# Performance work log

Hardware: AMD Instinct MI355X
Metric: run time of the kernel (lower is better)

## Reference

```python
import jax, jax.numpy as jnp
import numpy as np

D_MODEL = 1024
N_HEADS = 16
D_KV = 64
N_CONTEXT = 20
PASSAGE_LEN = 200
BSZ = 8
QLEN = 32
KLEN = N_CONTEXT * PASSAGE_LEN


def setup_inputs() -> dict:
    key = jax.random.key(0)
    ks = jax.random.split(key, 8)
    inp = {
        "input": jax.random.normal(ks[0], (BSZ, QLEN, D_MODEL), jnp.float32),
        "kv": jax.random.normal(ks[1], (BSZ, KLEN, D_MODEL), jnp.float32),
        "mask_add": jnp.zeros((BSZ, 1, 1, KLEN), jnp.float32),
        "mask_bool": jnp.ones((BSZ, 1, 1, KLEN), bool),
        "position_bias": jax.random.normal(ks[2], (1, N_HEADS, QLEN, KLEN), jnp.float32),
        "Wq": jax.random.normal(ks[3], (D_MODEL, N_HEADS * D_KV), jnp.float32) * 0.02,
        "Wk": jax.random.normal(ks[4], (D_MODEL, N_HEADS * D_KV), jnp.float32) * 0.02,
        "Wv": jax.random.normal(ks[5], (D_MODEL, N_HEADS * D_KV), jnp.float32) * 0.02,
        "Wo": jax.random.normal(ks[6], (N_HEADS * D_KV, D_MODEL), jnp.float32) * 0.02,
        "n_context": N_CONTEXT,
    }
    return inp


def reference(input, kv, mask_add, mask_bool, position_bias, Wq, Wk, Wv, Wo, n_context):
    b, qlen, dm = input.shape
    klen = kv.shape[1]
    H = position_bias.shape[1]
    dh = Wq.shape[1] // H
    # projections, [b, h, len, dh]
    q = (input @ Wq).reshape(b, qlen, H, dh).transpose(0, 2, 1, 3)
    k = (kv @ Wk).reshape(b, klen, H, dh).transpose(0, 2, 1, 3)
    v = (kv @ Wv).reshape(b, klen, H, dh).transpose(0, 2, 1, 3)
    # unscaled T5-style attention scores + additive mask + position bias
    scores = jnp.einsum('bhqd,bhkd->bhqk', q, k) + mask_add + position_bias
    attn = jax.nn.softmax(scores.astype(jnp.float32), axis=-1).astype(scores.dtype)
    # dropout p=0 (eval) -> identity
    out = jnp.einsum('bhqk,bhkd->bhqd', attn, v)
    out = out.transpose(0, 2, 1, 3).reshape(b, qlen, H * dh) @ Wo
    # collect_cross_attention(sum_over_tokens=True): masked avg of raw scores per context
    s = scores.reshape(b, H, qlen, n_context, -1)
    m = mask_bool.reshape(b, 1, 1, n_context, -1).astype(scores.dtype)
    collected = (s * m).sum(-1) / m.sum(-1)  # [b, H, qlen, n_context]
    return out, collected
```

## Files before the change

kernel.cpp:

```cpp
#include <hip/hip_runtime.h>
#include <stdint.h>

constexpr int DMODEL = 1024;
constexpr int NH     = 16;
constexpr int DHD    = 64;
constexpr int BS     = 8;
constexpr int QLEN   = 32;
constexpr int KLEN   = 4000;
constexpr int NCTX   = 20;
constexpr int PLEN   = 200;

typedef __bf16 bf16_t;
typedef bf16_t bf16x8 __attribute__((ext_vector_type(8)));
typedef float  f32x4  __attribute__((ext_vector_type(4)));

__device__ __forceinline__ uint16_t f2bf(float f) {
  uint32_t u = __float_as_uint(f);
  u += 0x7FFF + ((u >> 16) & 1);
  return (uint16_t)(u >> 16);
}

#define GLOAD_LDS16(gsrc, ldst) \
  __builtin_amdgcn_global_load_lds((const __attribute__((address_space(1))) void*)(gsrc), \
                                   (__attribute__((address_space(3))) void*)(ldst), 16, 0, 0)

__global__ void cast_inputs(const float* __restrict__ kv, const float* __restrict__ inp,
                            uint16_t* __restrict__ kv16, uint16_t* __restrict__ in16,
                            const uint32_t* __restrict__ maskw, int* __restrict__ flag) {
  if (blockIdx.x == 0 && threadIdx.x == 0)
    *flag = (maskw[0] == 0x01010101u) ? 1 : 0;
  const int NKV4 = (BS * KLEN * DMODEL) / 4;
  const int NIN4 = (BS * QLEN * DMODEL) / 4;
  const int total = NKV4 + NIN4;
  for (int i = blockIdx.x * blockDim.x + threadIdx.x; i < total; i += gridDim.x * blockDim.x) {
    float4 v; uint16_t* dst; int di;
    if (i < NKV4) { v = ((const float4*)kv)[i]; dst = kv16; di = i; }
    else          { v = ((const float4*)inp)[i - NKV4]; dst = in16; di = i - NKV4; }
    ushort4 o; o.x = f2bf(v.x); o.y = f2bf(v.y); o.z = f2bf(v.z); o.w = f2bf(v.w);
    ((ushort4*)dst)[di] = o;
  }
}

__global__ void wtrans(const float* __restrict__ w0, const float* __restrict__ w1,
                       const float* __restrict__ w2, const float* __restrict__ w3,
                       uint16_t* __restrict__ out) {
  __shared__ uint16_t sm[64][65];
  const float* W = (blockIdx.z == 0) ? w0 : (blockIdx.z == 1) ? w1 : (blockIdx.z == 2) ? w2 : w3;
  uint16_t* o = out + (size_t)blockIdx.z * DMODEL * DMODEL;
  int k0 = blockIdx.y * 64, n0 = blockIdx.x * 64;
  int t = threadIdx.x;
  for (int i = 0; i < 16; ++i) {
    int s = t + i * 256; int r = s >> 6, c = s & 63;
    sm[r][c] = f2bf(W[(size_t)(k0 + r) * DMODEL + n0 + c]);
  }
  __syncthreads();
  for (int i = 0; i < 16; ++i) {
    int s = t + i * 256; int r = s >> 6, c = s & 63;
    o[(size_t)(n0 + r) * DMODEL + k0 + c] = sm[c][r];
  }
}

template <int OUT_F32>
__global__ void __launch_bounds__(256) gemm_bt(const uint16_t* __restrict__ A,
                                               const uint16_t* __restrict__ Bt,
                                               void* __restrict__ Cv,
                                               int M, int N, int K) {
  __shared__ __align__(16) uint16_t As[128 * 32];
  __shared__ __align__(16) uint16_t Bs[64 * 32];
  const int m0 = blockIdx.x * 128, n0 = blockIdx.y * 64;
  const int tid = threadIdx.x, lane = tid & 63, wave = tid >> 6;
  const int wm = wave >> 1, wn = wave & 1;
  const int l15 = lane & 15, g = lane >> 4;
  const int sr = lane >> 2, sc = (lane & 3) * 8;
  const int c0 = wave * 3, c1 = c0 + 1, c2 = c0 + 2;
  f32x4 acc[4][2] = {};
  const int KT = K / 32;
  for (int kt = 0; kt < KT; ++kt) {
    __syncthreads();
#pragma unroll
    for (int cq = 0; cq < 3; ++cq) {
      const int c = wave * 3 + cq;
      if (c < 8)
        GLOAD_LDS16(A  + (size_t)(m0 + c * 16 + sr) * K + kt * 32 + sc, As + c * 512);
      else
        GLOAD_LDS16(Bt + (size_t)(n0 + (c - 8) * 16 + sr) * K + kt * 32 + sc, Bs + (c - 8) * 512);
    }
    __syncthreads();
    bf16x8 a[4], b[2];
#pragma unroll
    for (int i = 0; i < 4; ++i)
      a[i] = *(const bf16x8*)&As[(wm * 64 + i * 16 + l15) * 32 + g * 8];
#pragma unroll
    for (int j = 0; j < 2; ++j)
      b[j] = *(const bf16x8*)&Bs[(wn * 32 + j * 16 + l15) * 32 + g * 8];
#pragma unroll
    for (int i = 0; i < 4; ++i)
#pragma unroll
      for (int j = 0; j < 2; ++j)
        acc[i][j] = __builtin_amdgcn_mfma_f32_16x16x32_bf16(a[i], b[j], acc[i][j], 0, 0, 0);
  }
#pragma unroll
  for (int i = 0; i < 4; ++i)
#pragma unroll
    for (int j = 0; j < 2; ++j) {
      int row = m0 + wm * 64 + i * 16 + g * 4;
      int col = n0 + wn * 32 + j * 16 + l15;
      if (OUT_F32) {
        float* C = (float*)Cv;
#pragma unroll
        for (int r = 0; r < 4; ++r) C[(size_t)(row + r) * N + col] = acc[i][j][r];
      } else {
        uint16_t* C = (uint16_t*)Cv;
#pragma unroll
        for (int r = 0; r < 4; ++r) C[(size_t)(row + r) * N + col] = f2bf(acc[i][j][r]);
      }
    }
}

__global__ void __launch_bounds__(512) gemm_kv(const uint16_t* __restrict__ A,
                                               const uint16_t* __restrict__ Bt,
                                               uint16_t* __restrict__ kmat,
                                               uint16_t* __restrict__ vt) {
  __shared__ __align__(16) uint16_t smem[65536];
  const int orig = blockIdx.x;
  const int swz  = (orig & 7) * 125 + (orig >> 3);
  const int mb = swz >> 3, nb = swz & 7;
  const int m0 = mb * 256, n0 = nb * 256;
  const int tid = threadIdx.x, lane = tid & 63, wid = tid >> 6;
  const int wm = wid >> 2, wn = wid & 3;
  const int l15 = lane & 15, g = lane >> 4;
  const int l3 = lane >> 3, l7 = lane & 7;
  const int cg = (l7 ^ (l3 & 7)) * 8;

  f32x4 acc[8][4] = {};

#define ABASE(bf) (smem + (bf) * 32768)
#define BBASE(bf) (smem + (bf) * 32768 + 16384)

  auto STAGE = [&](int bf, int kt) {
    const int colg = kt * 64 + cg;
#pragma unroll
    for (int ia = 0; ia < 4; ++ia) {
      const int r0 = wid * 32 + ia * 8;
      GLOAD_LDS16(A + (size_t)(m0 + r0 + l3) * 1024 + colg, ABASE(bf) + r0 * 64);
    }
#pragma unroll
    for (int ib = 0; ib < 4; ++ib) {
      const int r0 = wid * 32 + ib * 8;
      GLOAD_LDS16(Bt + (size_t)(n0 + r0 + l3) * 1024 + colg, BBASE(bf) + r0 * 64);
    }
  };

  STAGE(0, 0);
  for (int kt = 0; kt < 16; ++kt) {
    const int bf = kt & 1;
    if (kt < 15) {
      STAGE(bf ^ 1, kt + 1);
      asm volatile("s_waitcnt vmcnt(8)" ::: "memory");
    } else {
      asm volatile("s_waitcnt vmcnt(0)" ::: "memory");
    }
    asm volatile("s_barrier" ::: "memory");
#pragma unroll
    for (int kk = 0; kk < 2; ++kk) {
      bf16x8 af[8], bb[4];
#pragma unroll
      for (int mi = 0; mi < 8; ++mi) {
        const int row = wm * 128 + mi * 16 + l15;
        const int gr = (kk * 4 + g) ^ (row & 7);
        af[mi] = *(const bf16x8*)&ABASE(bf)[row * 64 + gr * 8];
      }
#pragma unroll
      for (int ni = 0; ni < 4; ++ni) {
        const int row = wn * 64 + ni * 16 + l15;
        const int gr = (kk * 4 + g) ^ (row & 7);
        bb[ni] = *(const bf16x8*)&BBASE(bf)[row * 64 + gr * 8];
      }
#pragma unroll
      for (int mi = 0; mi < 8; ++mi)
#pragma unroll
        for (int ni = 0; ni < 4; ++ni)
          acc[mi][ni] = __builtin_amdgcn_mfma_f32_16x16x32_bf16(af[mi], bb[ni], acc[mi][ni], 0, 0, 0);
    }
    asm volatile("s_barrier" ::: "memory");
  }
#undef ABASE
#undef BBASE

  if (n0 < 1024) {
#pragma unroll
    for (int mi = 0; mi < 8; ++mi)
#pragma unroll
      for (int ni = 0; ni < 4; ++ni) {
        const int row = m0 + wm * 128 + mi * 16 + g * 4;
        const int col = n0 + wn * 64 + ni * 16 + l15;
#pragma unroll
        for (int r = 0; r < 4; ++r)
          kmat[(size_t)(row + r) * 1024 + col] = f2bf(acc[mi][ni][r]);
      }
  } else {
#pragma unroll
    for (int mi = 0; mi < 8; ++mi)
#pragma unroll
      for (int ni = 0; ni < 4; ++ni) {
        const int dd = wn * 64 + ni * 16 + l15;
        const int kk_tok = wm * 128 + mi * 16 + g * 4;
#pragma unroll
        for (int r = 0; r < 4; ++r)
          smem[dd * 256 + kk_tok + r] = f2bf(acc[mi][ni][r]);
      }
    __syncthreads();
    const int hbase = (n0 - 1024) >> 6;
#pragma unroll
    for (int it = 0; it < 16; ++it) {
      const int sp = it * 512 + tid;
      const int dd = sp >> 5, kk0 = (sp & 31) * 8;
      const int grow = m0 + kk0;
      const int b = grow / 4000, krel = grow - b * 4000;
      const int h = hbase + (dd >> 6), d = dd & 63;
      ulonglong2 v = *(const ulonglong2*)&smem[dd * 256 + kk0];
      *(ulonglong2*)&vt[(((size_t)(b * NH + h) * DHD + d) * KLEN) + krel] = v;
    }
  }
}

__global__ void __launch_bounds__(256) fused_attn(const uint16_t* __restrict__ Q,
                                                  const uint16_t* __restrict__ Km,
                                                  const uint16_t* __restrict__ Vt,
                                                  const float* __restrict__ mask_add,
                                                  const void* __restrict__ maskb,
                                                  const int* __restrict__ flag,
                                                  const float* __restrict__ bias,
                                                  float* __restrict__ part,
                                                  float* __restrict__ coll) {
  __shared__ __align__(16) uint16_t plds[4][32 * 32];
  const int kc = blockIdx.x, h = blockIdx.y, b = blockIdx.z;
  const int lane = threadIdx.x & 63, wave = threadIdx.x >> 6;
  const int l15 = lane & 15, g = lane >> 4;
  const int ctx = kc * 4 + wave;
  const int kbase = ctx * PLEN;
  const int fm = *flag;

  bf16x8 aq[2][2];
#pragma unroll
  for (int i = 0; i < 2; ++i)
#pragma unroll
    for (int ks = 0; ks < 2; ++ks)
      aq[i][ks] = *(const bf16x8*)&Q[(size_t)(b * QLEN + i * 16 + l15) * DMODEL + h * DHD + ks * 32 + g * 8];

  f32x4 o[2][4] = {};
  float mr[2][4], lr[2][4], cs[2][4];
#pragma unroll
  for (int i = 0; i < 2; ++i)
#pragma unroll
    for (int r = 0; r < 4; ++r) { mr[i][r] = -3e38f; lr[i][r] = 0.f; cs[i][r] = 0.f; }
  float cnt = 0.f;

  for (int t = 0; t < 7; ++t) {
    const int k0 = kbase + t * 32;
    bf16x8 kb[2][2];
#pragma unroll
    for (int j = 0; j < 2; ++j) {
      int kr = k0 + j * 16 + l15; if (kr > KLEN - 1) kr = KLEN - 1;
#pragma unroll
      for (int ks = 0; ks < 2; ++ks)
        kb[j][ks] = *(const bf16x8*)&Km[(size_t)(b * KLEN + kr) * DMODEL + h * DHD + ks * 32 + g * 8];
    }
    f32x4 sa[2][2] = {};
#pragma unroll
    for (int ks = 0; ks < 2; ++ks)
#pragma unroll
      for (int i = 0; i < 2; ++i)
#pragma unroll
        for (int j = 0; j < 2; ++j)
          sa[i][j] = __builtin_amdgcn_mfma_f32_16x16x32_bf16(aq[i][ks], kb[j][ks], sa[i][j], 0, 0, 0);

    int colc[2]; bool vd[2], vm[2]; float ma[2];
#pragma unroll
    for (int j = 0; j < 2; ++j) {
      int col = k0 + j * 16 + l15;
      vd[j] = (col < kbase + PLEN);
      int cc = col; if (cc > KLEN - 1) cc = KLEN - 1;
      colc[j] = cc;
      ma[j] = mask_add[b * KLEN + cc];
      bool mk = fm ? (((const uint8_t*)maskb)[b * KLEN + cc] != 0)
                   : (((const int*)maskb)[b * KLEN + cc] != 0);
      vm[j] = vd[j] && mk;
    }

    float sv[2][2][4];
    float tmax[2][4];
#pragma unroll
    for (int i = 0; i < 2; ++i)
#pragma unroll
      for (int r = 0; r < 4; ++r) {
        tmax[i][r] = -3e38f;
        const int q = i * 16 + g * 4 + r;
        const size_t brow = (size_t)(h * QLEN + q) * KLEN;
#pragma unroll
        for (int j = 0; j < 2; ++j) {
          float raw = sa[i][j][r] + ma[j] + bias[brow + colc[j]];
          cs[i][r] += vm[j] ? raw : 0.f;
          float x = vd[j] ? raw : -3e38f;
          sv[i][j][r] = x;
          tmax[i][r] = fmaxf(tmax[i][r], x);
        }
      }
#pragma unroll
    for (int j = 0; j < 2; ++j) cnt += vm[j] ? 1.f : 0.f;

#pragma unroll
    for (int i = 0; i < 2; ++i)
#pragma unroll
      for (int r = 0; r < 4; ++r) {
        float v = tmax[i][r];
        v = fmaxf(v, __shfl_xor(v, 1)); v = fmaxf(v, __shfl_xor(v, 2));
        v = fmaxf(v, __shfl_xor(v, 4)); v = fmaxf(v, __shfl_xor(v, 8));
        tmax[i][r] = v;
      }
    float scale[2][4];
#pragma unroll
    for (int i = 0; i < 2; ++i)
#pragma unroll
      for (int r = 0; r < 4; ++r) {
        float mn = fmaxf(mr[i][r], tmax[i][r]);
        scale[i][r] = __expf(mr[i][r] - mn);
        mr[i][r] = mn;
        lr[i][r] *= scale[i][r];
      }
#pragma unroll
    for (int i = 0; i < 2; ++i)
#pragma unroll
      for (int j2 = 0; j2 < 4; ++j2)
#pragma unroll
        for (int r = 0; r < 4; ++r)
          o[i][j2][r] *= scale[i][r];
#pragma unroll
    for (int i = 0; i < 2; ++i)
#pragma unroll
      for (int r = 0; r < 4; ++r) {
        const int q = i * 16 + g * 4 + r;
#pragma unroll
        for (int j = 0; j < 2; ++j) {
          float p = __expf(sv[i][j][r] - mr[i][r]);
          lr[i][r] += p;
          plds[wave][q * 32 + j * 16 + l15] = f2bf(p);
        }
      }
    bf16x8 ap[2];
#pragma unroll
    for (int i = 0; i < 2; ++i)
      ap[i] = *(const bf16x8*)&plds[wave][(i * 16 + l15) * 32 + g * 8];
    bf16x8 vb[4];
    int vc = k0 + g * 8; if (vc > KLEN - 8) vc = KLEN - 8;
#pragma unroll
    for (int j2 = 0; j2 < 4; ++j2)
      vb[j2] = *(const bf16x8*)&Vt[((size_t)((b * NH + h) * DHD + j2 * 16 + l15)) * KLEN + vc];
#pragma unroll
    for (int i = 0; i < 2; ++i)
#pragma unroll
      for (int j2 = 0; j2 < 4; ++j2)
        o[i][j2] = __builtin_amdgcn_mfma_f32_16x16x32_bf16(ap[i], vb[j2], o[i][j2], 0, 0, 0);
  }

#pragma unroll
  for (int i = 0; i < 2; ++i)
#pragma unroll
    for (int r = 0; r < 4; ++r) {
      float v = lr[i][r];
      v += __shfl_xor(v, 1); v += __shfl_xor(v, 2); v += __shfl_xor(v, 4); v += __shfl_xor(v, 8);
      lr[i][r] = v;
      float c = cs[i][r];
      c += __shfl_xor(c, 1); c += __shfl_xor(c, 2); c += __shfl_xor(c, 4); c += __shfl_xor(c, 8);
      cs[i][r] = c;
    }
  { float c = cnt; c += __shfl_xor(c, 1); c += __shfl_xor(c, 2); c += __shfl_xor(c, 4); c += __shfl_xor(c, 8); cnt = c; }

  float* pr = part + ((size_t)((b * NH + h) * NCTX + ctx)) * 32 * 72;
#pragma unroll
  for (int i = 0; i < 2; ++i)
#pragma unroll
    for (int j2 = 0; j2 < 4; ++j2)
#pragma unroll
      for (int r = 0; r < 4; ++r)
        pr[(i * 16 + g * 4 + r) * 72 + 8 + j2 * 16 + l15] = o[i][j2][r];
  if (l15 == 0) {
#pragma unroll
    for (int i = 0; i < 2; ++i)
#pragma unroll
      for (int r = 0; r < 4; ++r) {
        int q = i * 16 + g * 4 + r;
        pr[q * 72 + 0] = mr[i][r];
        pr[q * 72 + 1] = lr[i][r];
        coll[(((size_t)(b * NH + h)) * QLEN + q) * NCTX + ctx] = cs[i][r] / cnt;
      }
  }
}

__global__ void __launch_bounds__(256) combine_attn(const float* __restrict__ part,
                                                    uint16_t* __restrict__ ao16) {
  const int t = threadIdx.x;
  const int row = blockIdx.x * 16 + (t >> 4);
  const int ln = t & 15;
  const int bh = row >> 5, q = row & 31;
  const float* p0 = part + ((size_t)bh * 640 + q) * 72;
  float M = -3e38f;
#pragma unroll
  for (int c = 0; c < NCTX; ++c) M = fmaxf(M, p0[(size_t)c * 2304]);
  float Z = 0.f, o0 = 0.f, o1 = 0.f, o2 = 0.f, o3 = 0.f;
  const int d0 = ln * 4;
  for (int c = 0; c < NCTX; ++c) {
    const float* pc = p0 + (size_t)c * 2304;
    float e = __expf(pc[0] - M);
    Z += e * pc[1];
    float4 ov = *(const float4*)&pc[8 + d0];
    o0 += e * ov.x; o1 += e * ov.y; o2 += e * ov.z; o3 += e * ov.w;
  }
  float iz = 1.f / Z;
  const int b = bh >> 4, h = bh & 15;
  ushort4 w; w.x = f2bf(o0 * iz); w.y = f2bf(o1 * iz); w.z = f2bf(o2 * iz); w.w = f2bf(o3 * iz);
  *(ushort4*)&ao16[(size_t)(b * QLEN + q) * DMODEL + h * DHD + d0] = w;
}

extern "C" void kernel_launch(void* const* d_in, const int* in_sizes, int n_in,
                              void* d_out, int out_size, void* d_ws, size_t ws_size,
                              hipStream_t stream) {
  const float* input     = (const float*)d_in[0];
  const float* kv        = (const float*)d_in[1];
  const float* mask_add  = (const float*)d_in[2];
  const void*  mask_bool = d_in[3];
  const float* bias      = (const float*)d_in[4];
  const float* Wq        = (const float*)d_in[5];
  const float* Wk        = (const float*)d_in[6];
  const float* Wv        = (const float*)d_in[7];
  const float* Wo        = (const float*)d_in[8];
  float* out  = (float*)d_out;
  float* coll = out + (size_t)BS * QLEN * DMODEL;

  char* ws = (char*)d_ws;
  size_t off = 0;
  auto alloc = [&](size_t bytes) { char* p = ws + off; off += (bytes + 255) & ~(size_t)255; return p; };
  uint16_t* kv16 = (uint16_t*)alloc((size_t)BS * KLEN * DMODEL * 2);
  uint16_t* in16 = (uint16_t*)alloc((size_t)BS * QLEN * DMODEL * 2);
  uint16_t* wt   = (uint16_t*)alloc((size_t)4 * DMODEL * DMODEL * 2);
  uint16_t* q16  = (uint16_t*)alloc((size_t)BS * QLEN * DMODEL * 2);
  uint16_t* kmat = (uint16_t*)alloc((size_t)BS * KLEN * DMODEL * 2);
  uint16_t* vt   = (uint16_t*)alloc((size_t)BS * KLEN * DMODEL * 2);
  float*    part = (float*)   alloc((size_t)BS * NH * NCTX * 32 * 72 * 4);
  uint16_t* ao16 = (uint16_t*)alloc((size_t)BS * QLEN * DMODEL * 2);
  int*      flag = (int*)alloc(256);

  uint16_t* WqT  = wt;
  uint16_t* WkvT = wt + (size_t)DMODEL * DMODEL;
  uint16_t* WoT  = wt + (size_t)3 * DMODEL * DMODEL;

  cast_inputs<<<2048, 256, 0, stream>>>(kv, input, kv16, in16,
                                        (const uint32_t*)mask_bool, flag);
  wtrans<<<dim3(16, 16, 4), 256, 0, stream>>>(Wq, Wk, Wv, Wo, wt);
  gemm_bt<0><<<dim3(2, 16), 256, 0, stream>>>(in16, WqT, q16, BS * QLEN, DMODEL, DMODEL);
  gemm_kv<<<1000, 512, 0, stream>>>(kv16, WkvT, kmat, vt);
  fused_attn<<<dim3(5, NH, BS), 256, 0, stream>>>(q16, kmat, vt, mask_add, mask_bool, flag,
                                                  bias, part, coll);
  combine_attn<<<256, 256, 0, stream>>>(part, ao16);
  gemm_bt<1><<<dim3(2, 16), 256, 0, stream>>>(ao16, WoT, out, BS * QLEN, DMODEL, DMODEL);
}
```

Baseline: 287.8 us.

## Split each context across two waves and merge partial softmax in LDS

Each passage of 200 keys is now processed by two waves of 100 keys each, and the grid doubles from 5 to 10 blocks along the context axis. The two halves' running max, sum, output accumulators and masked score sums are merged through shared memory before one partial record per context is written. This targets the low parallelism and long serial key loop of the attention kernel, which had 640 blocks. The cost is extra shared memory, a block barrier and merge arithmetic, and the last tile of each half does work on padded columns.

```diff
diff --git a/kernel.cpp b/kernel.cpp
--- a/kernel.cpp
+++ b/kernel.cpp
@@ -72,7 +72,6 @@
   const int wm = wave >> 1, wn = wave & 1;
   const int l15 = lane & 15, g = lane >> 4;
   const int sr = lane >> 2, sc = (lane & 3) * 8;
-  const int c0 = wave * 3, c1 = c0 + 1, c2 = c0 + 2;
   f32x4 acc[4][2] = {};
   const int KT = K / 32;
   for (int kt = 0; kt < KT; ++kt) {
@@ -234,11 +233,14 @@
                                                   float* __restrict__ part,
                                                   float* __restrict__ coll) {
   __shared__ __align__(16) uint16_t plds[4][32 * 32];
+  __shared__ __align__(16) float mlds[4][32][72];
   const int kc = blockIdx.x, h = blockIdx.y, b = blockIdx.z;
   const int lane = threadIdx.x & 63, wave = threadIdx.x >> 6;
   const int l15 = lane & 15, g = lane >> 4;
-  const int ctx = kc * 4 + wave;
-  const int kbase = ctx * PLEN;
+  const int ctx = kc * 2 + (wave >> 1);
+  const int half = wave & 1;
+  const int kbase = ctx * PLEN + half * 100;
+  const int kend = kbase + 100;
   const int fm = *flag;
 
   bf16x8 aq[2][2];
@@ -256,7 +258,7 @@
     for (int r = 0; r < 4; ++r) { mr[i][r] = -3e38f; lr[i][r] = 0.f; cs[i][r] = 0.f; }
   float cnt = 0.f;
 
-  for (int t = 0; t < 7; ++t) {
+  for (int t = 0; t < 4; ++t) {
     const int k0 = kbase + t * 32;
     bf16x8 kb[2][2];
 #pragma unroll
@@ -279,7 +281,7 @@
 #pragma unroll
     for (int j = 0; j < 2; ++j) {
       int col = k0 + j * 16 + l15;
-      vd[j] = (col < kbase + PLEN);
+      vd[j] = (col < kend);
       int cc = col; if (cc > KLEN - 1) cc = KLEN - 1;
       colc[j] = cc;
       ma[j] = mask_add[b * KLEN + cc];
@@ -352,7 +354,7 @@
     for (int i = 0; i < 2; ++i)
       ap[i] = *(const bf16x8*)&plds[wave][(i * 16 + l15) * 32 + g * 8];
     bf16x8 vb[4];
-    int vc = k0 + g * 8; if (vc > KLEN - 8) vc = KLEN - 8;
+    const int vc = k0 + g * 8;
 #pragma unroll
     for (int j2 = 0; j2 < 4; ++j2)
       vb[j2] = *(const bf16x8*)&Vt[((size_t)((b * NH + h) * DHD + j2 * 16 + l15)) * KLEN + vc];
@@ -376,24 +378,49 @@
     }
   { float c = cnt; c += __shfl_xor(c, 1); c += __shfl_xor(c, 2); c += __shfl_xor(c, 4); c += __shfl_xor(c, 8); cnt = c; }
 
-  float* pr = part + ((size_t)((b * NH + h) * NCTX + ctx)) * 32 * 72;
 #pragma unroll
   for (int i = 0; i < 2; ++i)
 #pragma unroll
     for (int j2 = 0; j2 < 4; ++j2)
 #pragma unroll
       for (int r = 0; r < 4; ++r)
-        pr[(i * 16 + g * 4 + r) * 72 + 8 + j2 * 16 + l15] = o[i][j2][r];
+        mlds[wave][i * 16 + g * 4 + r][8 + j2 * 16 + l15] = o[i][j2][r];
   if (l15 == 0) {
 #pragma unroll
     for (int i = 0; i < 2; ++i)
 #pragma unroll
       for (int r = 0; r < 4; ++r) {
-        int q = i * 16 + g * 4 + r;
-        pr[q * 72 + 0] = mr[i][r];
-        pr[q * 72 + 1] = lr[i][r];
-        coll[(((size_t)(b * NH + h)) * QLEN + q) * NCTX + ctx] = cs[i][r] / cnt;
-      }
+        const int q = i * 16 + g * 4 + r;
+        mlds[wave][q][0] = mr[i][r];
+        mlds[wave][q][1] = lr[i][r];
+        mlds[wave][q][2] = cs[i][r];
+        mlds[wave][q][3] = cnt;
+      }
+  }
+  __syncthreads();
+  if ((wave & 1) == 0) {
+    const int q = lane >> 1, hp = lane & 1;
+    const float m0v = mlds[wave][q][0], m1v = mlds[wave + 1][q][0];
+    const float l0v = mlds[wave][q][1], l1v = mlds[wave + 1][q][1];
+    const float M = fmaxf(m0v, m1v);
+    const float s0 = __expf(m0v - M), s1 = __expf(m1v - M);
+    float* pr = part + ((size_t)((b * NH + h) * NCTX + ctx)) * 32 * 72 + q * 72;
+#pragma unroll
+    for (int d = 0; d < 32; d += 4) {
+      const int dd = hp * 32 + d;
+      float4 a = *(const float4*)&mlds[wave][q][8 + dd];
+      float4 c = *(const float4*)&mlds[wave + 1][q][8 + dd];
+      float4 o4; o4.x = s0 * a.x + s1 * c.x; o4.y = s0 * a.y + s1 * c.y;
+      o4.z = s0 * a.z + s1 * c.z; o4.w = s0 * a.w + s1 * c.w;
+      *(float4*)&pr[8 + dd] = o4;
+    }
+    if (hp == 0) {
+      pr[0] = M;
+      pr[1] = s0 * l0v + s1 * l1v;
+      const float csT  = mlds[wave][q][2] + mlds[wave + 1][q][2];
+      const float cntT = mlds[wave][q][3] + mlds[wave + 1][q][3];
+      coll[((size_t)(b * NH + h) * QLEN + q) * NCTX + ctx] = csT / cntT;
+    }
   }
 }
 
@@ -459,8 +486,8 @@
   wtrans<<<dim3(16, 16, 4), 256, 0, stream>>>(Wq, Wk, Wv, Wo, wt);
   gemm_bt<0><<<dim3(2, 16), 256, 0, stream>>>(in16, WqT, q16, BS * QLEN, DMODEL, DMODEL);
   gemm_kv<<<1000, 512, 0, stream>>>(kv16, WkvT, kmat, vt);
-  fused_attn<<<dim3(5, NH, BS), 256, 0, stream>>>(q16, kmat, vt, mask_add, mask_bool, flag,
-                                                  bias, part, coll);
+  fused_attn<<<dim3(10, NH, BS), 256, 0, stream>>>(q16, kmat, vt, mask_add, mask_bool, flag,
+                                                   bias, part, coll);
   combine_attn<<<256, 256, 0, stream>>>(part, ao16);
   gemm_bt<1><<<dim3(2, 16), 256, 0, stream>>>(ao16, WoT, out, BS * QLEN, DMODEL, DMODEL);
 }
```

Result: no change. 290.2 us (+0.8%).
